# Kernel optimization log

Measured on AMD Instinct MI355X. Metric: run time of the kernel, lower is better.

Reference implementation:

```python
import jax, jax.numpy as jnp
import numpy as np

N_AGENTS = 12
N_THREADS = 4096
DIM = 3
N_VEC = 4
HID = 64
INV_NF = 32
LAYERS = 2
N = N_THREADS * N_AGENTS


def _intra_graph_edges():
    # fully-connected directed edges within each env's agent graph
    i, j = np.meshgrid(np.arange(N_AGENTS), np.arange(N_AGENTS), indexing='ij')
    mask = i != j
    ri, ci = i[mask], j[mask]  # [132]
    off = (np.arange(N_THREADS) * N_AGENTS)[:, None]
    row = (ri[None, :] + off).reshape(-1).astype(np.int32)
    col = (ci[None, :] + off).reshape(-1).astype(np.int32)
    return jnp.asarray(row), jnp.asarray(col)


def setup_inputs() -> dict:
    key = jax.random.key(0)
    ks = jax.random.split(key, 16)
    s = 0.05
    row, col = _intra_graph_edges()
    return {
        'h0': jax.random.normal(ks[0], (N, INV_NF), jnp.float32),
        'x0': jax.random.normal(ks[1], (N, DIM, N_VEC), jnp.float32),
        'W_embed': jax.random.normal(ks[2], (INV_NF, HID), jnp.float32) * s,
        'b_embed': jnp.zeros((HID,), jnp.float32),
        'We1': jax.random.normal(ks[3], (LAYERS, 2 * HID + N_VEC, HID), jnp.float32) * s,
        'be1': jnp.zeros((LAYERS, HID), jnp.float32),
        'We2': jax.random.normal(ks[4], (LAYERS, HID, HID), jnp.float32) * s,
        'be2': jnp.zeros((LAYERS, HID), jnp.float32),
        'Wx': jax.random.normal(ks[5], (LAYERS, HID, N_VEC), jnp.float32) * s,
        'bx': jnp.zeros((LAYERS, N_VEC), jnp.float32),
        'Wh1': jax.random.normal(ks[6], (LAYERS, 2 * HID, HID), jnp.float32) * s,
        'bh1': jnp.zeros((LAYERS, HID), jnp.float32),
        'Wh2': jax.random.normal(ks[7], (LAYERS, HID, HID), jnp.float32) * s,
        'bh2': jnp.zeros((LAYERS, HID), jnp.float32),
        'w_act': jax.random.normal(ks[8], (N_VEC,), jnp.float32) * s,
        'log_std': jnp.full((DIM,), -0.5, jnp.float32),
        'row': row,
        'col': col,
    }


def reference(h0, x0, W_embed, b_embed, We1, be1, We2, be2, Wx, bx,
              Wh1, bh1, Wh2, bh2, w_act, log_std, row, col):
    silu = jax.nn.silu
    n = h0.shape[0]
    h = h0 @ W_embed + b_embed            # node embedding, [N, HID]
    x = x0                                 # equivariant features, [N, DIM, N_VEC]
    deg = jnp.maximum(jax.ops.segment_sum(jnp.ones_like(row, jnp.float32), row, num_segments=n), 1.0)
    for l in range(LAYERS):
        hi, hj = h[row], h[col]
        diff = x[row] - x[col]                        # [E, DIM, N_VEC]
        radial = jnp.sum(diff * diff, axis=1)          # [E, N_VEC]
        m = silu(jnp.concatenate([hi, hj, radial], -1) @ We1[l] + be1[l])
        m = silu(m @ We2[l] + be2[l])                  # edge messages [E, HID]
        wc = m @ Wx[l] + bx[l]                         # per-vector coord weights [E, N_VEC]
        x = x + jax.ops.segment_sum(diff * wc[:, None, :], row, num_segments=n) / deg[:, None, None]
        agg = jax.ops.segment_sum(m, row, num_segments=n)
        h = h + silu(jnp.concatenate([h, agg], -1) @ Wh1[l] + bh1[l]) @ Wh2[l] + bh2[l]
    mu = jnp.einsum('ndv,v->nd', x, w_act)             # act_net: Linear(N_VEC,1,bias=False)
    actions = mu                                        # deterministic: mode of Normal(mu, std)
    log_probs = jnp.broadcast_to(-log_std - 0.5 * jnp.log(2.0 * jnp.pi), mu.shape)
    actions = actions.reshape(N_THREADS, N_AGENTS, DIM)
    log_probs = log_probs.reshape(N_THREADS, N_AGENTS, DIM)
    return actions, log_probs
```

## Files before the change

### kernel.cpp

```cpp
#include <hip/hip_runtime.h>

#define NAG 12
#define NTH 4096
#define NEDGE 132
#define ENVW 4
#define LDB 72
#define LDT 20

typedef __bf16 bf16_8 __attribute__((ext_vector_type(8)));
typedef __bf16 bf16_4 __attribute__((ext_vector_type(4)));
typedef float  f32x4  __attribute__((ext_vector_type(4)));

#define MFMA(a,b,c) __builtin_amdgcn_mfma_f32_16x16x32_bf16((a),(b),(c),0,0,0)

#define WS_FRAGS 100
#define WS_BIAS_F32 25600
#define WS_BX_F32   27648
#define WS_BYTES 111104

__device__ __forceinline__ float silu_f(float z) {
    float e = __expf(-z);
    return z * __builtin_amdgcn_rcpf(1.0f + e);
}

__device__ __forceinline__ bf16_8 loadB64(const float* __restrict__ W, int kbase, int n, int q) {
    bf16_8 b;
    #pragma unroll
    for (int j = 0; j < 8; ++j) b[j] = (__bf16)W[(kbase + q*8 + j) * 64 + n];
    return b;
}

__device__ __forceinline__ bf16_8 packA8(const float* S) {
    f32x4 u = *(const f32x4*)S, v = *(const f32x4*)(S + 4);
    bf16_8 a;
    a[0]=(__bf16)u.x; a[1]=(__bf16)u.y; a[2]=(__bf16)u.z; a[3]=(__bf16)u.w;
    a[4]=(__bf16)v.x; a[5]=(__bf16)v.y; a[6]=(__bf16)v.z; a[7]=(__bf16)v.w;
    return a;
}

__global__ __launch_bounds__(64) void prep_frags(
    const float* __restrict__ W_embed, const float* __restrict__ We1,
    const float* __restrict__ We2, const float* __restrict__ Wh1,
    const float* __restrict__ Wh2,
    const float* __restrict__ be1, const float* __restrict__ be2,
    const float* __restrict__ bh1, const float* __restrict__ bh2,
    const float* __restrict__ bx, __bf16* __restrict__ wsb)
{
    const int f = blockIdx.x, lane = threadIdx.x;
    const int q = lane >> 4, n16 = lane & 15;
    float* wsf = (float*)wsb;
    if (f < WS_FRAGS) {
        const float* src; int kbase, nbase;
        if (f < 4) { src = W_embed; kbase = 0; nbase = f * 16; }
        else {
            int g0 = f - 4, l = g0 / 48, r = g0 % 48;
            if      (r < 8)  { int nt=r>>1, kh=r&1;            src = We1 + l*NEDGE*64; kbase = kh*32;      nbase = nt*16; }
            else if (r < 16) { int rr=r-8,  nt=rr>>1, kh=rr&1; src = We1 + l*NEDGE*64; kbase = 64 + kh*32; nbase = nt*16; }
            else if (r < 24) { int rr=r-16, nt=rr>>1, kh=rr&1; src = We2 + l*64*64;    kbase = kh*32;      nbase = nt*16; }
            else if (r < 40) { int rr=r-24, nt=rr>>2, ks=rr&3; src = Wh1 + l*128*64;   kbase = ks*32;      nbase = nt*16; }
            else             { int rr=r-40, nt=rr>>1, kh=rr&1; src = Wh2 + l*64*64;    kbase = kh*32;      nbase = nt*16; }
        }
        bf16_8 b = loadB64(src, kbase, nbase + n16, q);
        *(bf16_8*)(wsb + (size_t)f * 512 + lane * 8) = b;
    } else if (f < WS_FRAGS + 8) {
        int f2 = f - WS_FRAGS, l = f2 >> 2, w = f2 & 3;
        const float* src = (w == 0 ? be1 : w == 1 ? be2 : w == 2 ? bh1 : bh2) + l * 64;
        f32x4 v = { src[n16], src[16 + n16], src[32 + n16], src[48 + n16] };
        *(f32x4*)(wsf + WS_BIAS_F32 + ((size_t)(l*4 + w) * 64 + lane) * 4) = v;
    } else {
        #pragma unroll
        for (int l = 0; l < 2; ++l)
            wsf[WS_BX_F32 + l*64 + lane] = (n16 < 4) ? bx[l*4 + n16] : 0.f;
    }
}

template<bool WS>
__device__ __forceinline__ bf16_8 frg(const __bf16* __restrict__ wsb, int fid,
                                      const float* __restrict__ src, int kbase, int n, int lane) {
    if (WS) return *(const bf16_8*)(wsb + (size_t)fid * 512 + lane * 8);
    else    return loadB64(src, kbase, n, (lane >> 4));
}

template<bool WS>
__global__ void __launch_bounds__(64) egnn11(
    const float* __restrict__ h0, const float* __restrict__ x0,
    const float* __restrict__ W_embed, const float* __restrict__ b_embed,
    const float* __restrict__ We1, const float* __restrict__ be1,
    const float* __restrict__ We2, const float* __restrict__ be2,
    const float* __restrict__ Wx, const float* __restrict__ bx,
    const float* __restrict__ Wh1, const float* __restrict__ bh1,
    const float* __restrict__ Wh2, const float* __restrict__ bh2,
    const float* __restrict__ w_act, const float* __restrict__ log_std,
    const __bf16* __restrict__ wsb, float* __restrict__ out)
{
    __shared__ __align__(16) __bf16 sh  [ENVW][NAG * LDB];
    __shared__ __align__(16) __bf16 sHa [ENVW][NAG * LDB];
    __shared__ __align__(16) __bf16 sHb [ENVW][NAG * LDB];
    __shared__ __align__(16) __bf16 mstT[ENVW][64 * LDT];
    __shared__ __align__(16) float  sx  [ENVW][NAG * 16];
    __shared__ __align__(16) __bf16 sWcB[ENVW][NEDGE * 4];
    __shared__ __align__(16) float  sWb [4 * 64];

    const int lane = threadIdx.x;
    const int q = lane >> 4, n16 = lane & 15;
    const int rowA = (n16 < NAG) ? n16 : (NAG - 1);
    const int env0 = blockIdx.x * ENVW;
    const float* wsf = (const float*)wsb;

    if (lane < NAG * 3) {
        int d = lane % 3;
        float lp = -log_std[d] - 0.9189385332046727f;
        #pragma unroll
        for (int ep = 0; ep < ENVW; ++ep)
            out[NTH * NAG * 3 + (env0 + ep) * (NAG*3) + lane] = lp;
    }

    #pragma unroll
    for (int p = 0; p < (ENVW * 144 + 63) / 64; ++p) {
        int idx = p * 64 + lane;
        if (idx < ENVW * 144) {
            int ep = idx / 144, r2 = idx - ep * 144;
            sx[ep][(r2 / 12) * 16 + r2 % 12] = x0[(env0) * NAG * 12 + idx];
        }
    }

    f32x4 hC[ENVW][4];
    {
        bf16_8 a[ENVW];
        #pragma unroll
        for (int ep = 0; ep < ENVW; ++ep)
            a[ep] = packA8(h0 + ((env0 + ep) * NAG + rowA) * 32 + q * 8);
        #pragma unroll
        for (int nt = 0; nt < 4; ++nt) {
            bf16_8 b = frg<WS>(wsb, nt, W_embed, 0, nt*16 + n16, lane);
            float bias = b_embed[nt*16 + n16];
            #pragma unroll
            for (int ep = 0; ep < ENVW; ++ep) {
                f32x4 acc = {0.f,0.f,0.f,0.f};
                acc = MFMA(a[ep], b, acc);
                #pragma unroll
                for (int r = 0; r < 4; ++r) acc[r] += bias;
                hC[ep][nt] = acc;
            }
        }
        #pragma unroll
        for (int ep = 0; ep < ENVW; ++ep)
            #pragma unroll
            for (int nt = 0; nt < 4; ++nt)
                #pragma unroll
                for (int r = 0; r < 4; ++r) {
                    int row = q*4 + r;
                    if (row < NAG) sh[ep][row*LDB + nt*16 + n16] = (__bf16)hC[ep][nt][r];
                }
    }

    #pragma unroll 1
    for (int l = 0; l < 2; ++l) {
        const float* We1l = We1 + l * NEDGE * 64;
        const float* be1l = be1 + l * 64;
        const float* be2l = be2 + l * 64;
        const float* Wxl  = Wx  + l * 64 * 4;
        const float* bxl  = bx  + l * 4;
        const float* We2l = We2 + l * 64 * 64;
        const float* Wh1l = Wh1 + l * 128 * 64;
        const float* bh1l = bh1 + l * 64;
        const float* Wh2l = Wh2 + l * 64 * 64;
        const float* bh2l = bh2 + l * 64;
        const int L = 4 + l * 48;

        f32x4 be1q, be2q, bh1q, bh2q;
        float bxv;
        if (WS) {
            const float* bb = wsf + WS_BIAS_F32 + (size_t)(l*4) * 256 + lane * 4;
            be1q = *(const f32x4*)(bb);
            be2q = *(const f32x4*)(bb + 256);
            bh1q = *(const f32x4*)(bb + 512);
            bh2q = *(const f32x4*)(bb + 768);
            bxv  = wsf[WS_BX_F32 + l*64 + lane];
        } else {
            #pragma unroll
            for (int nt = 0; nt < 4; ++nt) {
                be1q[nt] = be1l[nt*16+n16]; be2q[nt] = be2l[nt*16+n16];
                bh1q[nt] = bh1l[nt*16+n16]; bh2q[nt] = bh2l[nt*16+n16];
            }
            bxv = (n16 < 4) ? bxl[n16] : 0.f;
        }

        {
            bf16_8 a0[ENVW], a1[ENVW];
            #pragma unroll
            for (int ep = 0; ep < ENVW; ++ep) {
                a0[ep] = *(const bf16_8*)(sh[ep] + rowA*LDB + q*8);
                a1[ep] = *(const bf16_8*)(sh[ep] + rowA*LDB + 32 + q*8);
            }
            #pragma unroll
            for (int nt = 0; nt < 4; ++nt) {
                bf16_8 b0 = frg<WS>(wsb, L+nt*2+0,   We1l, 0,  nt*16+n16, lane);
                bf16_8 b1 = frg<WS>(wsb, L+nt*2+1,   We1l, 32, nt*16+n16, lane);
                bf16_8 c0 = frg<WS>(wsb, L+8+nt*2+0, We1l, 64, nt*16+n16, lane);
                bf16_8 c1 = frg<WS>(wsb, L+8+nt*2+1, We1l, 96, nt*16+n16, lane);
                #pragma unroll
                for (int ep = 0; ep < ENVW; ++ep) {
                    f32x4 aA = {0.f,0.f,0.f,0.f}, aB = {0.f,0.f,0.f,0.f};
                    aA = MFMA(a0[ep], b0, aA); aA = MFMA(a1[ep], b1, aA);
                    aB = MFMA(a0[ep], c0, aB); aB = MFMA(a1[ep], c1, aB);
                    #pragma unroll
                    for (int r = 0; r < 4; ++r) {
                        int row = q*4 + r;
                        if (row < NAG) {
                            sHa[ep][row*LDB + nt*16+n16] = (__bf16)(aA[r] + be1q[nt]);
                            sHb[ep][row*LDB + nt*16+n16] = (__bf16)aB[r];
                        }
                    }
                }
            }
        }
        #pragma unroll
        for (int p = 0; p < 4; ++p) sWb[p*64 + lane] = We1l[(128+p)*64 + lane];

        float agg[ENVW][NAG];
        #pragma unroll
        for (int ep = 0; ep < ENVW; ++ep)
            #pragma unroll
            for (int i = 0; i < NAG; ++i) agg[ep][i] = 0.f;
        bf16_8 w2f[4][2], wxf[2];
        #pragma unroll
        for (int nt = 0; nt < 4; ++nt) {
            w2f[nt][0] = frg<WS>(wsb, L+16+nt*2+0, We2l, 0,  nt*16+n16, lane);
            w2f[nt][1] = frg<WS>(wsb, L+16+nt*2+1, We2l, 32, nt*16+n16, lane);
        }
        #pragma unroll
        for (int kh = 0; kh < 2; ++kh) {
            bf16_8 b;
            #pragma unroll
            for (int j2 = 0; j2 < 8; ++j2)
                b[j2] = (n16 < 4) ? (__bf16)Wxl[(kh*32 + q*8 + j2)*4 + n16] : (__bf16)0.f;
            wxf[kh] = b;
        }

        #pragma unroll
        for (int t = 0; t < 9; ++t) {
            const int e  = t*16 + n16;
            const int ec = (e < NEDGE) ? e : (NEDGE - 1);
            const int i  = ec / 11;
            const int jj = ec - i * 11;
            const int j  = jj + (jj >= i);
            bf16_8 af[ENVW][2];
            #pragma unroll
            for (int ep = 0; ep < ENVW; ++ep) {
                f32x4 rd = {0.f,0.f,0.f,0.f};
                #pragma unroll
                for (int d = 0; d < 3; ++d) {
                    f32x4 xi = *(const f32x4*)(sx[ep] + i*16 + d*4);
                    f32x4 xj = *(const f32x4*)(sx[ep] + j*16 + d*4);
                    f32x4 df = xi - xj;
                    rd += df * df;
                }
                #pragma unroll
                for (int kh = 0; kh < 2; ++kh) {
                    const int cb = kh*32 + q*8;
                    bf16_8 ha = *(const bf16_8*)(sHa[ep] + i*LDB + cb);
                    bf16_8 hb = *(const bf16_8*)(sHb[ep] + j*LDB + cb);
                    f32x4 wr0 = {0.f,0.f,0.f,0.f}, wr1 = {0.f,0.f,0.f,0.f};
                    #pragma unroll
                    for (int v = 0; v < 4; ++v) {
                        f32x4 wa = *(const f32x4*)(sWb + v*64 + cb);
                        f32x4 wb = *(const f32x4*)(sWb + v*64 + cb + 4);
                        wr0 += rd[v] * wa; wr1 += rd[v] * wb;
                    }
                    bf16_8 a;
                    #pragma unroll
                    for (int c = 0; c < 4; ++c)
                        a[c]   = (__bf16)silu_f((float)ha[c]   + (float)hb[c]   + wr0[c]);
                    #pragma unroll
                    for (int c = 0; c < 4; ++c)
                        a[4+c] = (__bf16)silu_f((float)ha[4+c] + (float)hb[4+c] + wr1[c]);
                    af[ep][kh] = a;
                }
            }
            #pragma unroll
            for (int ep = 0; ep < ENVW; ++ep) {
                __bf16* mT = &mstT[ep][0];
                #pragma unroll
                for (int nt = 0; nt < 4; ++nt) {
                    f32x4 acc = {0.f,0.f,0.f,0.f};
                    acc = MFMA(af[ep][0], w2f[nt][0], acc);
                    acc = MFMA(af[ep][1], w2f[nt][1], acc);
                    bf16_4 mv;
                    #pragma unroll
                    for (int r = 0; r < 4; ++r) mv[r] = (__bf16)silu_f(acc[r] + be2q[nt]);
                    *(bf16_4*)(mT + (nt*16 + n16)*LDT + q*4) = mv;
                }
            }
            #pragma unroll
            for (int ep = 0; ep < ENVW; ++ep) {
                const __bf16* mT = &mstT[ep][0];
                bf16_8 aw0, aw1;
                #pragma unroll
                for (int j2 = 0; j2 < 8; ++j2) {
                    aw0[j2] = mT[(q*8 + j2)*LDT + n16];
                    aw1[j2] = mT[(32 + q*8 + j2)*LDT + n16];
                }
                f32x4 acc = {0.f,0.f,0.f,0.f};
                acc = MFMA(aw0, wxf[0], acc);
                acc = MFMA(aw1, wxf[1], acc);
                if (n16 < 4) {
                    #pragma unroll
                    for (int r = 0; r < 4; ++r) {
                        int row = t*16 + q*4 + r;
                        if (row < NEDGE) sWcB[ep][row*4 + n16] = (__bf16)(acc[r] + bxv);
                    }
                }
            }
            #pragma unroll
            for (int ep = 0; ep < ENVW; ++ep) {
                const __bf16* mT = &mstT[ep][0];
                bf16_4 c0 = *(const bf16_4*)(mT + lane*LDT + 0);
                #pragma unroll
                for (int el = 0; el < 4; ++el) agg[ep][(t*16 + el)/11] += (float)c0[el];
                if (t < 8) {
                    bf16_4 c1 = *(const bf16_4*)(mT + lane*LDT + 4);
                    bf16_4 c2 = *(const bf16_4*)(mT + lane*LDT + 8);
                    bf16_4 c3 = *(const bf16_4*)(mT + lane*LDT + 12);
                    #pragma unroll
                    for (int el = 0; el < 4; ++el) {
                        agg[ep][(t*16 + 4  + el)/11] += (float)c1[el];
                        agg[ep][(t*16 + 8  + el)/11] += (float)c2[el];
                        agg[ep][(t*16 + 12 + el)/11] += (float)c3[el];
                    }
                }
            }
        }
        #pragma unroll
        for (int ep = 0; ep < ENVW; ++ep)
            #pragma unroll
            for (int i = 0; i < NAG; ++i) sHb[ep][i*LDB + lane] = (__bf16)agg[ep][i];

        float xn[ENVW][3];
        #pragma unroll
        for (int p = 0; p < 3; ++p) {
            int idx = p*64 + lane;
            int xi = idx / 12, dv = idx % 12, v = dv & 3;
            bool act = idx < 144;
            int xic = act ? xi : 0;
            #pragma unroll
            for (int ep = 0; ep < ENVW; ++ep) {
                float xiv = sx[ep][xic*16 + dv];
                float acc = 0.f;
                #pragma unroll
                for (int j2 = 0; j2 < NAG; ++j2) {
                    int e2 = xic*11 + j2 - (j2 > xic ? 1 : 0);
                    e2 = (e2 < NEDGE) ? e2 : (NEDGE - 1);
                    float term = (xiv - sx[ep][j2*16 + dv]) * (float)sWcB[ep][e2*4 + v];
                    acc += (j2 == xic) ? 0.f : term;
                }
                xn[ep][p] = act ? (xiv + acc * (1.0f / 11.0f)) : 0.f;
            }
        }
        {
            bf16_8 ah0[ENVW], ah1[ENVW], ag0[ENVW], ag1[ENVW];
            #pragma unroll
            for (int ep = 0; ep < ENVW; ++ep) {
                ah0[ep] = *(const bf16_8*)(sh[ep]  + rowA*LDB + q*8);
                ah1[ep] = *(const bf16_8*)(sh[ep]  + rowA*LDB + 32 + q*8);
                ag0[ep] = *(const bf16_8*)(sHb[ep] + rowA*LDB + q*8);
                ag1[ep] = *(const bf16_8*)(sHb[ep] + rowA*LDB + 32 + q*8);
            }
            #pragma unroll
            for (int nt = 0; nt < 4; ++nt) {
                bf16_8 b0 = frg<WS>(wsb, L+24+nt*4+0, Wh1l, 0,  nt*16+n16, lane);
                bf16_8 b1 = frg<WS>(wsb, L+24+nt*4+1, Wh1l, 32, nt*16+n16, lane);
                bf16_8 b2 = frg<WS>(wsb, L+24+nt*4+2, Wh1l, 64, nt*16+n16, lane);
                bf16_8 b3 = frg<WS>(wsb, L+24+nt*4+3, Wh1l, 96, nt*16+n16, lane);
                #pragma unroll
                for (int ep = 0; ep < ENVW; ++ep) {
                    f32x4 acc = {0.f,0.f,0.f,0.f};
                    acc = MFMA(ah0[ep], b0, acc); acc = MFMA(ah1[ep], b1, acc);
                    acc = MFMA(ag0[ep], b2, acc); acc = MFMA(ag1[ep], b3, acc);
                    #pragma unroll
                    for (int r = 0; r < 4; ++r) {
                        int row = q*4 + r;
                        if (row < NAG) sHa[ep][row*LDB + nt*16+n16] = (__bf16)silu_f(acc[r] + bh1q[nt]);
                    }
                }
            }
        }
        #pragma unroll
        for (int p = 0; p < 3; ++p) {
            int idx = p*64 + lane;
            if (idx < 144) {
                #pragma unroll
                for (int ep = 0; ep < ENVW; ++ep)
                    sx[ep][(idx/12)*16 + idx%12] = xn[ep][p];
            }
        }
        {
            bf16_8 at0[ENVW], at1[ENVW];
            #pragma unroll
            for (int ep = 0; ep < ENVW; ++ep) {
                at0[ep] = *(const bf16_8*)(sHa[ep] + rowA*LDB + q*8);
                at1[ep] = *(const bf16_8*)(sHa[ep] + rowA*LDB + 32 + q*8);
            }
            #pragma unroll
            for (int nt = 0; nt < 4; ++nt) {
                bf16_8 b0 = frg<WS>(wsb, L+40+nt*2+0, Wh2l, 0,  nt*16+n16, lane);
                bf16_8 b1 = frg<WS>(wsb, L+40+nt*2+1, Wh2l, 32, nt*16+n16, lane);
                #pragma unroll
                for (int ep = 0; ep < ENVW; ++ep) {
                    f32x4 acc = {0.f,0.f,0.f,0.f};
                    acc = MFMA(at0[ep], b0, acc);
                    acc = MFMA(at1[ep], b1, acc);
                    #pragma unroll
                    for (int r = 0; r < 4; ++r) hC[ep][nt][r] += acc[r] + bh2q[nt];
                }
            }
            #pragma unroll
            for (int ep = 0; ep < ENVW; ++ep)
                #pragma unroll
                for (int nt = 0; nt < 4; ++nt)
                    #pragma unroll
                    for (int r = 0; r < 4; ++r) {
                        int row = q*4 + r;
                        if (row < NAG) sh[ep][row*LDB + nt*16+n16] = (__bf16)hC[ep][nt][r];
                    }
        }
    }

    if (lane < NAG * 3) {
        int i = lane / 3, d = lane - i * 3;
        #pragma unroll
        for (int ep = 0; ep < ENVW; ++ep) {
            float mu = 0.f;
            #pragma unroll
            for (int v = 0; v < 4; ++v) mu += sx[ep][i*16 + d*4 + v] * w_act[v];
            out[(env0 + ep) * (NAG*3) + lane] = mu;
        }
    }
}

extern "C" void kernel_launch(void* const* d_in, const int* in_sizes, int n_in,
                              void* d_out, int out_size, void* d_ws, size_t ws_size,
                              hipStream_t stream) {
    const float* h0   = (const float*)d_in[0];
    const float* x0   = (const float*)d_in[1];
    const float* Wem  = (const float*)d_in[2];
    const float* bem  = (const float*)d_in[3];
    const float* We1  = (const float*)d_in[4];
    const float* be1  = (const float*)d_in[5];
    const float* We2  = (const float*)d_in[6];
    const float* be2  = (const float*)d_in[7];
    const float* Wx   = (const float*)d_in[8];
    const float* bx   = (const float*)d_in[9];
    const float* Wh1  = (const float*)d_in[10];
    const float* bh1  = (const float*)d_in[11];
    const float* Wh2  = (const float*)d_in[12];
    const float* bh2  = (const float*)d_in[13];
    const float* wact = (const float*)d_in[14];
    const float* lstd = (const float*)d_in[15];
    float* out = (float*)d_out;

    if (ws_size >= (size_t)WS_BYTES) {
        prep_frags<<<dim3(WS_FRAGS + 9), dim3(64), 0, stream>>>(
            Wem, We1, We2, Wh1, Wh2, be1, be2, bh1, bh2, bx, (__bf16*)d_ws);
        egnn11<true><<<dim3(NTH / ENVW), dim3(64), 0, stream>>>(
            h0, x0, Wem, bem, We1, be1, We2, be2, Wx, bx,
            Wh1, bh1, Wh2, bh2, wact, lstd, (const __bf16*)d_ws, out);
    } else {
        egnn11<false><<<dim3(NTH / ENVW), dim3(64), 0, stream>>>(
            h0, x0, Wem, bem, We1, be1, We2, be2, Wx, bx,
            Wh1, bh1, Wh2, bh2, wact, lstd, nullptr, out);
    }
}
```

Baseline: 247.3 us.

## Pack four independent waves per block, each handling two environments

```diff
diff --git a/kernel.cpp b/kernel.cpp
--- a/kernel.cpp
+++ b/kernel.cpp
@@ -3,7 +3,8 @@
 #define NAG 12
 #define NTH 4096
 #define NEDGE 132
-#define ENVW 4
+#define ENVW 2
+#define NWAVE 4
 #define LDB 72
 #define LDT 20
 
@@ -82,7 +83,7 @@
 }
 
 template<bool WS>
-__global__ void __launch_bounds__(64) egnn11(
+__global__ void __launch_bounds__(64 * NWAVE) egnn11(
     const float* __restrict__ h0, const float* __restrict__ x0,
     const float* __restrict__ W_embed, const float* __restrict__ b_embed,
     const float* __restrict__ We1, const float* __restrict__ be1,
@@ -93,18 +94,20 @@
     const float* __restrict__ w_act, const float* __restrict__ log_std,
     const __bf16* __restrict__ wsb, float* __restrict__ out)
 {
-    __shared__ __align__(16) __bf16 sh  [ENVW][NAG * LDB];
-    __shared__ __align__(16) __bf16 sHa [ENVW][NAG * LDB];
-    __shared__ __align__(16) __bf16 sHb [ENVW][NAG * LDB];
-    __shared__ __align__(16) __bf16 mstT[ENVW][64 * LDT];
-    __shared__ __align__(16) float  sx  [ENVW][NAG * 16];
-    __shared__ __align__(16) __bf16 sWcB[ENVW][NEDGE * 4];
-    __shared__ __align__(16) float  sWb [4 * 64];
-
-    const int lane = threadIdx.x;
+    __shared__ __align__(16) __bf16 sh  [NWAVE][ENVW][NAG * LDB];
+    __shared__ __align__(16) __bf16 sHa [NWAVE][ENVW][NAG * LDB];
+    __shared__ __align__(16) __bf16 sHb [NWAVE][ENVW][NAG * LDB];
+    __shared__ __align__(16) __bf16 mstT[NWAVE][ENVW][64 * LDT];
+    __shared__ __align__(16) float  sx  [NWAVE][ENVW][NAG * 16];
+    __shared__ __align__(16) __bf16 sWcB[NWAVE][ENVW][NEDGE * 4];
+    __shared__ __align__(16) float  sWb [NWAVE][4 * 64];
+
+    const int tid  = threadIdx.x;
+    const int wv   = tid >> 6;
+    const int lane = tid & 63;
     const int q = lane >> 4, n16 = lane & 15;
     const int rowA = (n16 < NAG) ? n16 : (NAG - 1);
-    const int env0 = blockIdx.x * ENVW;
+    const int env0 = (blockIdx.x * NWAVE + wv) * ENVW;
     const float* wsf = (const float*)wsb;
 
     if (lane < NAG * 3) {
@@ -120,7 +123,7 @@
         int idx = p * 64 + lane;
         if (idx < ENVW * 144) {
             int ep = idx / 144, r2 = idx - ep * 144;
-            sx[ep][(r2 / 12) * 16 + r2 % 12] = x0[(env0) * NAG * 12 + idx];
+            sx[wv][ep][(r2 / 12) * 16 + r2 % 12] = x0[(env0) * NAG * 12 + idx];
         }
     }
 
@@ -150,7 +153,7 @@
                 #pragma unroll
                 for (int r = 0; r < 4; ++r) {
                     int row = q*4 + r;
-                    if (row < NAG) sh[ep][row*LDB + nt*16 + n16] = (__bf16)hC[ep][nt][r];
+                    if (row < NAG) sh[wv][ep][row*LDB + nt*16 + n16] = (__bf16)hC[ep][nt][r];
                 }
     }
 
@@ -190,8 +193,8 @@
             bf16_8 a0[ENVW], a1[ENVW];
             #pragma unroll
             for (int ep = 0; ep < ENVW; ++ep) {
-                a0[ep] = *(const bf16_8*)(sh[ep] + rowA*LDB + q*8);
-                a1[ep] = *(const bf16_8*)(sh[ep] + rowA*LDB + 32 + q*8);
+                a0[ep] = *(const bf16_8*)(sh[wv][ep] + rowA*LDB + q*8);
+                a1[ep] = *(const bf16_8*)(sh[wv][ep] + rowA*LDB + 32 + q*8);
             }
             #pragma unroll
             for (int nt = 0; nt < 4; ++nt) {
@@ -208,15 +211,15 @@
                     for (int r = 0; r < 4; ++r) {
                         int row = q*4 + r;
                         if (row < NAG) {
-                            sHa[ep][row*LDB + nt*16+n16] = (__bf16)(aA[r] + be1q[nt]);
-                            sHb[ep][row*LDB + nt*16+n16] = (__bf16)aB[r];
+                            sHa[wv][ep][row*LDB + nt*16+n16] = (__bf16)(aA[r] + be1q[nt]);
+                            sHb[wv][ep][row*LDB + nt*16+n16] = (__bf16)aB[r];
                         }
                     }
                 }
             }
         }
         #pragma unroll
-        for (int p = 0; p < 4; ++p) sWb[p*64 + lane] = We1l[(128+p)*64 + lane];
+        for (int p = 0; p < 4; ++p) sWb[wv][p*64 + lane] = We1l[(128+p)*64 + lane];
 
         float agg[ENVW][NAG];
         #pragma unroll
@@ -251,21 +254,21 @@
                 f32x4 rd = {0.f,0.f,0.f,0.f};
                 #pragma unroll
                 for (int d = 0; d < 3; ++d) {
-                    f32x4 xi = *(const f32x4*)(sx[ep] + i*16 + d*4);
-                    f32x4 xj = *(const f32x4*)(sx[ep] + j*16 + d*4);
+                    f32x4 xi = *(const f32x4*)(sx[wv][ep] + i*16 + d*4);
+                    f32x4 xj = *(const f32x4*)(sx[wv][ep] + j*16 + d*4);
                     f32x4 df = xi - xj;
                     rd += df * df;
                 }
                 #pragma unroll
                 for (int kh = 0; kh < 2; ++kh) {
                     const int cb = kh*32 + q*8;
-                    bf16_8 ha = *(const bf16_8*)(sHa[ep] + i*LDB + cb);
-                    bf16_8 hb = *(const bf16_8*)(sHb[ep] + j*LDB + cb);
+                    bf16_8 ha = *(const bf16_8*)(sHa[wv][ep] + i*LDB + cb);
+                    bf16_8 hb = *(const bf16_8*)(sHb[wv][ep] + j*LDB + cb);
                     f32x4 wr0 = {0.f,0.f,0.f,0.f}, wr1 = {0.f,0.f,0.f,0.f};
                     #pragma unroll
                     for (int v = 0; v < 4; ++v) {
-                        f32x4 wa = *(const f32x4*)(sWb + v*64 + cb);
-                        f32x4 wb = *(const f32x4*)(sWb + v*64 + cb + 4);
+                        f32x4 wa = *(const f32x4*)(sWb[wv] + v*64 + cb);
+                        f32x4 wb = *(const f32x4*)(sWb[wv] + v*64 + cb + 4);
                         wr0 += rd[v] * wa; wr1 += rd[v] * wb;
                     }
                     bf16_8 a;
@@ -280,7 +283,7 @@
             }
             #pragma unroll
             for (int ep = 0; ep < ENVW; ++ep) {
-                __bf16* mT = &mstT[ep][0];
+                __bf16* mT = &mstT[wv][ep][0];
                 #pragma unroll
                 for (int nt = 0; nt < 4; ++nt) {
                     f32x4 acc = {0.f,0.f,0.f,0.f};
@@ -294,7 +297,7 @@
             }
             #pragma unroll
             for (int ep = 0; ep < ENVW; ++ep) {
-                const __bf16* mT = &mstT[ep][0];
+                const __bf16* mT = &mstT[wv][ep][0];
                 bf16_8 aw0, aw1;
                 #pragma unroll
                 for (int j2 = 0; j2 < 8; ++j2) {
@@ -308,13 +311,13 @@
                     #pragma unroll
                     for (int r = 0; r < 4; ++r) {
                         int row = t*16 + q*4 + r;
-                        if (row < NEDGE) sWcB[ep][row*4 + n16] = (__bf16)(acc[r] + bxv);
-                    }
-                }
-            }
-            #pragma unroll
-            for (int ep = 0; ep < ENVW; ++ep) {
-                const __bf16* mT = &mstT[ep][0];
+                        if (row < NEDGE) sWcB[wv][ep][row*4 + n16] = (__bf16)(acc[r] + bxv);
+                    }
+                }
+            }
+            #pragma unroll
+            for (int ep = 0; ep < ENVW; ++ep) {
+                const __bf16* mT = &mstT[wv][ep][0];
                 bf16_4 c0 = *(const bf16_4*)(mT + lane*LDT + 0);
                 #pragma unroll
                 for (int el = 0; el < 4; ++el) agg[ep][(t*16 + el)/11] += (float)c0[el];
@@ -334,7 +337,7 @@
         #pragma unroll
         for (int ep = 0; ep < ENVW; ++ep)
             #pragma unroll
-            for (int i = 0; i < NAG; ++i) sHb[ep][i*LDB + lane] = (__bf16)agg[ep][i];
+            for (int i = 0; i < NAG; ++i) sHb[wv][ep][i*LDB + lane] = (__bf16)agg[ep][i];
 
         float xn[ENVW][3];
         #pragma unroll
@@ -345,13 +348,13 @@
             int xic = act ? xi : 0;
             #pragma unroll
             for (int ep = 0; ep < ENVW; ++ep) {
-                float xiv = sx[ep][xic*16 + dv];
+                float xiv = sx[wv][ep][xic*16 + dv];
                 float acc = 0.f;
                 #pragma unroll
                 for (int j2 = 0; j2 < NAG; ++j2) {
                     int e2 = xic*11 + j2 - (j2 > xic ? 1 : 0);
                     e2 = (e2 < NEDGE) ? e2 : (NEDGE - 1);
-                    float term = (xiv - sx[ep][j2*16 + dv]) * (float)sWcB[ep][e2*4 + v];
+                    float term = (xiv - sx[wv][ep][j2*16 + dv]) * (float)sWcB[wv][ep][e2*4 + v];
                     acc += (j2 == xic) ? 0.f : term;
                 }
                 xn[ep][p] = act ? (xiv + acc * (1.0f / 11.0f)) : 0.f;
@@ -361,10 +364,10 @@
             bf16_8 ah0[ENVW], ah1[ENVW], ag0[ENVW], ag1[ENVW];
             #pragma unroll
             for (int ep = 0; ep < ENVW; ++ep) {
-                ah0[ep] = *(const bf16_8*)(sh[ep]  + rowA*LDB + q*8);
-                ah1[ep] = *(const bf16_8*)(sh[ep]  + rowA*LDB + 32 + q*8);
-                ag0[ep] = *(const bf16_8*)(sHb[ep] + rowA*LDB + q*8);
-                ag1[ep] = *(const bf16_8*)(sHb[ep] + rowA*LDB + 32 + q*8);
+                ah0[ep] = *(const bf16_8*)(sh[wv][ep]  + rowA*LDB + q*8);
+                ah1[ep] = *(const bf16_8*)(sh[wv][ep]  + rowA*LDB + 32 + q*8);
+                ag0[ep] = *(const bf16_8*)(sHb[wv][ep] + rowA*LDB + q*8);
+                ag1[ep] = *(const bf16_8*)(sHb[wv][ep] + rowA*LDB + 32 + q*8);
             }
             #pragma unroll
             for (int nt = 0; nt < 4; ++nt) {
@@ -380,7 +383,7 @@
                     #pragma unroll
                     for (int r = 0; r < 4; ++r) {
                         int row = q*4 + r;
-                        if (row < NAG) sHa[ep][row*LDB + nt*16+n16] = (__bf16)silu_f(acc[r] + bh1q[nt]);
+                        if (row < NAG) sHa[wv][ep][row*LDB + nt*16+n16] = (__bf16)silu_f(acc[r] + bh1q[nt]);
                     }
                 }
             }
@@ -391,15 +394,15 @@
             if (idx < 144) {
                 #pragma unroll
                 for (int ep = 0; ep < ENVW; ++ep)
-                    sx[ep][(idx/12)*16 + idx%12] = xn[ep][p];
+                    sx[wv][ep][(idx/12)*16 + idx%12] = xn[ep][p];
             }
         }
         {
             bf16_8 at0[ENVW], at1[ENVW];
             #pragma unroll
             for (int ep = 0; ep < ENVW; ++ep) {
-                at0[ep] = *(const bf16_8*)(sHa[ep] + rowA*LDB + q*8);
-                at1[ep] = *(const bf16_8*)(sHa[ep] + rowA*LDB + 32 + q*8);
+                at0[ep] = *(const bf16_8*)(sHa[wv][ep] + rowA*LDB + q*8);
+                at1[ep] = *(const bf16_8*)(sHa[wv][ep] + rowA*LDB + 32 + q*8);
             }
             #pragma unroll
             for (int nt = 0; nt < 4; ++nt) {
@@ -421,7 +424,7 @@
                     #pragma unroll
                     for (int r = 0; r < 4; ++r) {
                         int row = q*4 + r;
-                        if (row < NAG) sh[ep][row*LDB + nt*16+n16] = (__bf16)hC[ep][nt][r];
+                        if (row < NAG) sh[wv][ep][row*LDB + nt*16+n16] = (__bf16)hC[ep][nt][r];
                     }
         }
     }
@@ -432,7 +435,7 @@
         for (int ep = 0; ep < ENVW; ++ep) {
             float mu = 0.f;
             #pragma unroll
-            for (int v = 0; v < 4; ++v) mu += sx[ep][i*16 + d*4 + v] * w_act[v];
+            for (int v = 0; v < 4; ++v) mu += sx[wv][ep][i*16 + d*4 + v] * w_act[v];
             out[(env0 + ep) * (NAG*3) + lane] = mu;
         }
     }
@@ -462,11 +465,11 @@
     if (ws_size >= (size_t)WS_BYTES) {
         prep_frags<<<dim3(WS_FRAGS + 9), dim3(64), 0, stream>>>(
             Wem, We1, We2, Wh1, Wh2, be1, be2, bh1, bh2, bx, (__bf16*)d_ws);
-        egnn11<true><<<dim3(NTH / ENVW), dim3(64), 0, stream>>>(
+        egnn11<true><<<dim3(NTH / (ENVW * NWAVE)), dim3(64 * NWAVE), 0, stream>>>(
             h0, x0, Wem, bem, We1, be1, We2, be2, Wx, bx,
             Wh1, bh1, Wh2, bh2, wact, lstd, (const __bf16*)d_ws, out);
     } else {
-        egnn11<false><<<dim3(NTH / ENVW), dim3(64), 0, stream>>>(
+        egnn11<false><<<dim3(NTH / (ENVW * NWAVE)), dim3(64 * NWAVE), 0, stream>>>(
             h0, x0, Wem, bem, We1, be1, We2, be2, Wx, bx,
             Wh1, bh1, Wh2, bh2, wact, lstd, nullptr, out);
     }
```

After: 222.1 us. 10.2% less time.

## Split each block's work across two waves and aggregate messages via MFMA

Applied to the files above, without the earlier changes.

```diff
diff --git a/kernel.cpp b/kernel.cpp
--- a/kernel.cpp
+++ b/kernel.cpp
@@ -3,7 +3,8 @@
 #define NAG 12
 #define NTH 4096
 #define NEDGE 132
-#define ENVW 4
+#define ENVW 2
+#define WPB 2
 #define LDB 72
 #define LDT 20
 
@@ -13,10 +14,10 @@
 
 #define MFMA(a,b,c) __builtin_amdgcn_mfma_f32_16x16x32_bf16((a),(b),(c),0,0,0)
 
-#define WS_FRAGS 100
-#define WS_BIAS_F32 25600
-#define WS_BX_F32   27648
-#define WS_BYTES 111104
+#define WS_FRAGS 109
+#define WS_BIAS_F32 27904
+#define WS_BX_F32   29952
+#define WS_BYTES 120320
 
 __device__ __forceinline__ float silu_f(float z) {
     float e = __expf(-z);
@@ -32,6 +33,13 @@
 
 __device__ __forceinline__ bf16_8 packA8(const float* S) {
     f32x4 u = *(const f32x4*)S, v = *(const f32x4*)(S + 4);
+    bf16_8 a;
+    a[0]=(__bf16)u.x; a[1]=(__bf16)u.y; a[2]=(__bf16)u.z; a[3]=(__bf16)u.w;
+    a[4]=(__bf16)v.x; a[5]=(__bf16)v.y; a[6]=(__bf16)v.z; a[7]=(__bf16)v.w;
+    return a;
+}
+
+__device__ __forceinline__ bf16_8 packA8v(f32x4 u, f32x4 v) {
     bf16_8 a;
     a[0]=(__bf16)u.x; a[1]=(__bf16)u.y; a[2]=(__bf16)u.z; a[3]=(__bf16)u.w;
     a[4]=(__bf16)v.x; a[5]=(__bf16)v.y; a[6]=(__bf16)v.z; a[7]=(__bf16)v.w;
@@ -49,7 +57,7 @@
     const int f = blockIdx.x, lane = threadIdx.x;
     const int q = lane >> 4, n16 = lane & 15;
     float* wsf = (float*)wsb;
-    if (f < WS_FRAGS) {
+    if (f < 100) {
         const float* src; int kbase, nbase;
         if (f < 4) { src = W_embed; kbase = 0; nbase = f * 16; }
         else {
@@ -62,6 +70,16 @@
         }
         bf16_8 b = loadB64(src, kbase, nbase + n16, q);
         *(bf16_8*)(wsb + (size_t)f * 512 + lane * 8) = b;
+    } else if (f < WS_FRAGS) {
+        int t = f - 100;
+        bf16_8 b;
+        #pragma unroll
+        for (int j = 0; j < 8; ++j) {
+            int k = q * 8 + j;
+            int e = t * 16 + k;
+            b[j] = (k < 16 && e < NEDGE && (e / 11) == n16) ? (__bf16)1.0f : (__bf16)0.0f;
+        }
+        *(bf16_8*)(wsb + (size_t)f * 512 + lane * 8) = b;
     } else if (f < WS_FRAGS + 8) {
         int f2 = f - WS_FRAGS, l = f2 >> 2, w = f2 & 3;
         const float* src = (w == 0 ? be1 : w == 1 ? be2 : w == 2 ? bh1 : bh2) + l * 64;
@@ -82,7 +100,7 @@
 }
 
 template<bool WS>
-__global__ void __launch_bounds__(64) egnn11(
+__global__ void __launch_bounds__(64 * WPB) egnn15(
     const float* __restrict__ h0, const float* __restrict__ x0,
     const float* __restrict__ W_embed, const float* __restrict__ b_embed,
     const float* __restrict__ We1, const float* __restrict__ be1,
@@ -96,42 +114,46 @@
     __shared__ __align__(16) __bf16 sh  [ENVW][NAG * LDB];
     __shared__ __align__(16) __bf16 sHa [ENVW][NAG * LDB];
     __shared__ __align__(16) __bf16 sHb [ENVW][NAG * LDB];
-    __shared__ __align__(16) __bf16 mstT[ENVW][64 * LDT];
+    __shared__ __align__(16) __bf16 mst [WPB][ENVW][64 * LDT];
+    __shared__ __align__(16) float  sAg [WPB][ENVW][NAG * 64];
     __shared__ __align__(16) float  sx  [ENVW][NAG * 16];
     __shared__ __align__(16) __bf16 sWcB[ENVW][NEDGE * 4];
     __shared__ __align__(16) float  sWb [4 * 64];
 
-    const int lane = threadIdx.x;
+    const int tid  = threadIdx.x;
+    const int wv   = tid >> 6;
+    const int lane = tid & 63;
     const int q = lane >> 4, n16 = lane & 15;
     const int rowA = (n16 < NAG) ? n16 : (NAG - 1);
     const int env0 = blockIdx.x * ENVW;
     const float* wsf = (const float*)wsb;
 
-    if (lane < NAG * 3) {
-        int d = lane % 3;
+    if (tid < NAG * 3) {
+        int d = tid % 3;
         float lp = -log_std[d] - 0.9189385332046727f;
         #pragma unroll
         for (int ep = 0; ep < ENVW; ++ep)
-            out[NTH * NAG * 3 + (env0 + ep) * (NAG*3) + lane] = lp;
+            out[NTH * NAG * 3 + (env0 + ep) * (NAG*3) + tid] = lp;
     }
 
     #pragma unroll
-    for (int p = 0; p < (ENVW * 144 + 63) / 64; ++p) {
-        int idx = p * 64 + lane;
+    for (int p = 0; p < 3; ++p) {
+        int idx = p * 128 + tid;
         if (idx < ENVW * 144) {
             int ep = idx / 144, r2 = idx - ep * 144;
             sx[ep][(r2 / 12) * 16 + r2 % 12] = x0[(env0) * NAG * 12 + idx];
         }
     }
 
-    f32x4 hC[ENVW][4];
+    f32x4 hC[ENVW][2];
     {
         bf16_8 a[ENVW];
         #pragma unroll
         for (int ep = 0; ep < ENVW; ++ep)
             a[ep] = packA8(h0 + ((env0 + ep) * NAG + rowA) * 32 + q * 8);
         #pragma unroll
-        for (int nt = 0; nt < 4; ++nt) {
+        for (int nt2 = 0; nt2 < 2; ++nt2) {
+            int nt = wv * 2 + nt2;
             bf16_8 b = frg<WS>(wsb, nt, W_embed, 0, nt*16 + n16, lane);
             float bias = b_embed[nt*16 + n16];
             #pragma unroll
@@ -140,19 +162,20 @@
                 acc = MFMA(a[ep], b, acc);
                 #pragma unroll
                 for (int r = 0; r < 4; ++r) acc[r] += bias;
-                hC[ep][nt] = acc;
+                hC[ep][nt2] = acc;
             }
         }
         #pragma unroll
         for (int ep = 0; ep < ENVW; ++ep)
             #pragma unroll
-            for (int nt = 0; nt < 4; ++nt)
+            for (int nt2 = 0; nt2 < 2; ++nt2)
                 #pragma unroll
                 for (int r = 0; r < 4; ++r) {
                     int row = q*4 + r;
-                    if (row < NAG) sh[ep][row*LDB + nt*16 + n16] = (__bf16)hC[ep][nt][r];
-                }
-    }
+                    if (row < NAG) sh[ep][row*LDB + (wv*2+nt2)*16 + n16] = (__bf16)hC[ep][nt2][r];
+                }
+    }
+    __syncthreads();
 
     #pragma unroll 1
     for (int l = 0; l < 2; ++l) {
@@ -168,20 +191,28 @@
         const float* bh2l = bh2 + l * 64;
         const int L = 4 + l * 48;
 
-        f32x4 be1q, be2q, bh1q, bh2q;
-        float bxv;
+        f32x4 be2q;
+        float be1s[2], bh1s[2], bh2s[2], bxv;
         if (WS) {
             const float* bb = wsf + WS_BIAS_F32 + (size_t)(l*4) * 256 + lane * 4;
-            be1q = *(const f32x4*)(bb);
             be2q = *(const f32x4*)(bb + 256);
-            bh1q = *(const f32x4*)(bb + 512);
-            bh2q = *(const f32x4*)(bb + 768);
-            bxv  = wsf[WS_BX_F32 + l*64 + lane];
+            #pragma unroll
+            for (int nt2 = 0; nt2 < 2; ++nt2) {
+                int nt = wv*2 + nt2;
+                be1s[nt2] = bb[nt];
+                bh1s[nt2] = bb[512 + nt];
+                bh2s[nt2] = bb[768 + nt];
+            }
+            bxv = wsf[WS_BX_F32 + l*64 + lane];
         } else {
             #pragma unroll
-            for (int nt = 0; nt < 4; ++nt) {
-                be1q[nt] = be1l[nt*16+n16]; be2q[nt] = be2l[nt*16+n16];
-                bh1q[nt] = bh1l[nt*16+n16]; bh2q[nt] = bh2l[nt*16+n16];
+            for (int nt = 0; nt < 4; ++nt) be2q[nt] = be2l[nt*16+n16];
+            #pragma unroll
+            for (int nt2 = 0; nt2 < 2; ++nt2) {
+                int nt = wv*2 + nt2;
+                be1s[nt2] = be1l[nt*16+n16];
+                bh1s[nt2] = bh1l[nt*16+n16];
+                bh2s[nt2] = bh2l[nt*16+n16];
             }
             bxv = (n16 < 4) ? bxl[n16] : 0.f;
         }
@@ -194,7 +225,8 @@
                 a1[ep] = *(const bf16_8*)(sh[ep] + rowA*LDB + 32 + q*8);
             }
             #pragma unroll
-            for (int nt = 0; nt < 4; ++nt) {
+            for (int nt2 = 0; nt2 < 2; ++nt2) {
+                int nt = wv*2 + nt2;
                 bf16_8 b0 = frg<WS>(wsb, L+nt*2+0,   We1l, 0,  nt*16+n16, lane);
                 bf16_8 b1 = frg<WS>(wsb, L+nt*2+1,   We1l, 32, nt*16+n16, lane);
                 bf16_8 c0 = frg<WS>(wsb, L+8+nt*2+0, We1l, 64, nt*16+n16, lane);
@@ -208,7 +240,7 @@
                     for (int r = 0; r < 4; ++r) {
                         int row = q*4 + r;
                         if (row < NAG) {
-                            sHa[ep][row*LDB + nt*16+n16] = (__bf16)(aA[r] + be1q[nt]);
+                            sHa[ep][row*LDB + nt*16+n16] = (__bf16)(aA[r] + be1s[nt2]);
                             sHb[ep][row*LDB + nt*16+n16] = (__bf16)aB[r];
                         }
                     }
@@ -216,13 +248,17 @@
             }
         }
         #pragma unroll
-        for (int p = 0; p < 4; ++p) sWb[p*64 + lane] = We1l[(128+p)*64 + lane];
-
-        float agg[ENVW][NAG];
+        for (int p2 = 0; p2 < 2; ++p2) {
+            int p = wv*2 + p2;
+            sWb[p*64 + lane] = We1l[(128+p)*64 + lane];
+        }
+        __syncthreads();
+
+        f32x4 aggC[ENVW][4];
         #pragma unroll
         for (int ep = 0; ep < ENVW; ++ep)
             #pragma unroll
-            for (int i = 0; i < NAG; ++i) agg[ep][i] = 0.f;
+            for (int nt = 0; nt < 4; ++nt) aggC[ep][nt] = (f32x4){0.f,0.f,0.f,0.f};
         bf16_8 w2f[4][2], wxf[2];
         #pragma unroll
         for (int nt = 0; nt < 4; ++nt) {
@@ -238,14 +274,14 @@
             wxf[kh] = b;
         }
 
-        #pragma unroll
-        for (int t = 0; t < 9; ++t) {
+        #pragma unroll 1
+        for (int t = (wv ? 4 : 0); t < (wv ? 9 : 4); ++t) {
             const int e  = t*16 + n16;
             const int ec = (e < NEDGE) ? e : (NEDGE - 1);
             const int i  = ec / 11;
             const int jj = ec - i * 11;
             const int j  = jj + (jj >= i);
-            bf16_8 af[ENVW][2];
+            f32x4 rdv[ENVW];
             #pragma unroll
             for (int ep = 0; ep < ENVW; ++ep) {
                 f32x4 rd = {0.f,0.f,0.f,0.f};
@@ -256,17 +292,26 @@
                     f32x4 df = xi - xj;
                     rd += df * df;
                 }
-                #pragma unroll
-                for (int kh = 0; kh < 2; ++kh) {
-                    const int cb = kh*32 + q*8;
+                rdv[ep] = rd;
+            }
+            bf16_8 af[ENVW][2];
+            #pragma unroll
+            for (int kh = 0; kh < 2; ++kh) {
+                const int cb = kh*32 + q*8;
+                f32x4 wa[4], wb[4];
+                #pragma unroll
+                for (int v = 0; v < 4; ++v) {
+                    wa[v] = *(const f32x4*)(sWb + v*64 + cb);
+                    wb[v] = *(const f32x4*)(sWb + v*64 + cb + 4);
+                }
+                #pragma unroll
+                for (int ep = 0; ep < ENVW; ++ep) {
                     bf16_8 ha = *(const bf16_8*)(sHa[ep] + i*LDB + cb);
                     bf16_8 hb = *(const bf16_8*)(sHb[ep] + j*LDB + cb);
                     f32x4 wr0 = {0.f,0.f,0.f,0.f}, wr1 = {0.f,0.f,0.f,0.f};
                     #pragma unroll
                     for (int v = 0; v < 4; ++v) {
-                        f32x4 wa = *(const f32x4*)(sWb + v*64 + cb);
-                        f32x4 wb = *(const f32x4*)(sWb + v*64 + cb + 4);
-                        wr0 += rd[v] * wa; wr1 += rd[v] * wb;
+                        wr0 += rdv[ep][v] * wa[v]; wr1 += rdv[ep][v] * wb[v];
                     }
                     bf16_8 a;
                     #pragma unroll
@@ -280,7 +325,7 @@
             }
             #pragma unroll
             for (int ep = 0; ep < ENVW; ++ep) {
-                __bf16* mT = &mstT[ep][0];
+                __bf16* mT = &mst[wv][ep][0];
                 #pragma unroll
                 for (int nt = 0; nt < 4; ++nt) {
                     f32x4 acc = {0.f,0.f,0.f,0.f};
@@ -294,7 +339,7 @@
             }
             #pragma unroll
             for (int ep = 0; ep < ENVW; ++ep) {
-                const __bf16* mT = &mstT[ep][0];
+                const __bf16* mT = &mst[wv][ep][0];
                 bf16_8 aw0, aw1;
                 #pragma unroll
                 for (int j2 = 0; j2 < 8; ++j2) {
@@ -312,34 +357,44 @@
                     }
                 }
             }
-            #pragma unroll
-            for (int ep = 0; ep < ENVW; ++ep) {
-                const __bf16* mT = &mstT[ep][0];
-                bf16_4 c0 = *(const bf16_4*)(mT + lane*LDT + 0);
-                #pragma unroll
-                for (int el = 0; el < 4; ++el) agg[ep][(t*16 + el)/11] += (float)c0[el];
-                if (t < 8) {
-                    bf16_4 c1 = *(const bf16_4*)(mT + lane*LDT + 4);
-                    bf16_4 c2 = *(const bf16_4*)(mT + lane*LDT + 8);
-                    bf16_4 c3 = *(const bf16_4*)(mT + lane*LDT + 12);
-                    #pragma unroll
-                    for (int el = 0; el < 4; ++el) {
-                        agg[ep][(t*16 + 4  + el)/11] += (float)c1[el];
-                        agg[ep][(t*16 + 8  + el)/11] += (float)c2[el];
-                        agg[ep][(t*16 + 12 + el)/11] += (float)c3[el];
-                    }
+            bf16_8 sfr;
+            if (WS) {
+                sfr = *(const bf16_8*)(wsb + (size_t)(100 + t) * 512 + lane * 8);
+            } else {
+                #pragma unroll
+                for (int j2 = 0; j2 < 8; ++j2) {
+                    int k = q*8 + j2, e2 = t*16 + k;
+                    sfr[j2] = (k < 16 && e2 < NEDGE && (e2 / 11) == n16) ? (__bf16)1.0f : (__bf16)0.0f;
+                }
+            }
+            #pragma unroll
+            for (int ep = 0; ep < ENVW; ++ep) {
+                const __bf16* mT = &mst[wv][ep][0];
+                #pragma unroll
+                for (int nt = 0; nt < 4; ++nt) {
+                    bf16_8 mb;
+                    #pragma unroll
+                    for (int c = 0; c < 8; ++c) mb[c] = (__bf16)0.f;
+                    if (q < 2) mb = *(const bf16_8*)(mT + (nt*16 + n16)*LDT + q*8);
+                    aggC[ep][nt] = MFMA(sfr, mb, aggC[ep][nt]);
                 }
             }
         }
         #pragma unroll
         for (int ep = 0; ep < ENVW; ++ep)
             #pragma unroll
-            for (int i = 0; i < NAG; ++i) sHb[ep][i*LDB + lane] = (__bf16)agg[ep][i];
-
-        float xn[ENVW][3];
-        #pragma unroll
-        for (int p = 0; p < 3; ++p) {
-            int idx = p*64 + lane;
+            for (int nt = 0; nt < 4; ++nt)
+                #pragma unroll
+                for (int r = 0; r < 4; ++r) {
+                    int row = q*4 + r;
+                    if (row < NAG) sAg[wv][ep][row*64 + nt*16+n16] = aggC[ep][nt][r];
+                }
+        __syncthreads();
+
+        float xn[ENVW][2];
+        #pragma unroll
+        for (int p = 0; p < 2; ++p) {
+            int idx = p*128 + tid;
             int xi = idx / 12, dv = idx % 12, v = dv & 3;
             bool act = idx < 144;
             int xic = act ? xi : 0;
@@ -361,13 +416,20 @@
             bf16_8 ah0[ENVW], ah1[ENVW], ag0[ENVW], ag1[ENVW];
             #pragma unroll
             for (int ep = 0; ep < ENVW; ++ep) {
-                ah0[ep] = *(const bf16_8*)(sh[ep]  + rowA*LDB + q*8);
-                ah1[ep] = *(const bf16_8*)(sh[ep]  + rowA*LDB + 32 + q*8);
-                ag0[ep] = *(const bf16_8*)(sHb[ep] + rowA*LDB + q*8);
-                ag1[ep] = *(const bf16_8*)(sHb[ep] + rowA*LDB + 32 + q*8);
-            }
-            #pragma unroll
-            for (int nt = 0; nt < 4; ++nt) {
+                ah0[ep] = *(const bf16_8*)(sh[ep] + rowA*LDB + q*8);
+                ah1[ep] = *(const bf16_8*)(sh[ep] + rowA*LDB + 32 + q*8);
+                const float* g0 = sAg[0][ep] + rowA*64;
+                const float* g1 = sAg[1][ep] + rowA*64;
+                f32x4 u0 = *(const f32x4*)(g0 + q*8)      + *(const f32x4*)(g1 + q*8);
+                f32x4 v0 = *(const f32x4*)(g0 + q*8 + 4)  + *(const f32x4*)(g1 + q*8 + 4);
+                f32x4 u1 = *(const f32x4*)(g0 + 32 + q*8) + *(const f32x4*)(g1 + 32 + q*8);
+                f32x4 v1 = *(const f32x4*)(g0 + 36 + q*8) + *(const f32x4*)(g1 + 36 + q*8);
+                ag0[ep] = packA8v(u0, v0);
+                ag1[ep] = packA8v(u1, v1);
+            }
+            #pragma unroll
+            for (int nt2 = 0; nt2 < 2; ++nt2) {
+                int nt = wv*2 + nt2;
                 bf16_8 b0 = frg<WS>(wsb, L+24+nt*4+0, Wh1l, 0,  nt*16+n16, lane);
                 bf16_8 b1 = frg<WS>(wsb, L+24+nt*4+1, Wh1l, 32, nt*16+n16, lane);
                 bf16_8 b2 = frg<WS>(wsb, L+24+nt*4+2, Wh1l, 64, nt*16+n16, lane);
@@ -380,14 +442,16 @@
                     #pragma unroll
                     for (int r = 0; r < 4; ++r) {
                         int row = q*4 + r;
-                        if (row < NAG) sHa[ep][row*LDB + nt*16+n16] = (__bf16)silu_f(acc[r] + bh1q[nt]);
+                        if (row < NAG) sHa[ep][row*LDB + nt*16+n16] = (__bf16)silu_f(acc[r] + bh1s[nt2]);
                     }
                 }
             }
         }
-        #pragma unroll
-        for (int p = 0; p < 3; ++p) {
-            int idx = p*64 + lane;
+        __syncthreads();
+
+        #pragma unroll
+        for (int p = 0; p < 2; ++p) {
+            int idx = p*128 + tid;
             if (idx < 144) {
                 #pragma unroll
                 for (int ep = 0; ep < ENVW; ++ep)
@@ -402,7 +466,8 @@
                 at1[ep] = *(const bf16_8*)(sHa[ep] + rowA*LDB + 32 + q*8);
             }
             #pragma unroll
-            for (int nt = 0; nt < 4; ++nt) {
+            for (int nt2 = 0; nt2 < 2; ++nt2) {
+                int nt = wv*2 + nt2;
                 bf16_8 b0 = frg<WS>(wsb, L+40+nt*2+0, Wh2l, 0,  nt*16+n16, lane);
                 bf16_8 b1 = frg<WS>(wsb, L+40+nt*2+1, Wh2l, 32, nt*16+n16, lane);
                 #pragma unroll
@@ -411,29 +476,30 @@
                     acc = MFMA(at0[ep], b0, acc);
                     acc = MFMA(at1[ep], b1, acc);
                     #pragma unroll
-                    for (int r = 0; r < 4; ++r) hC[ep][nt][r] += acc[r] + bh2q[nt];
+                    for (int r = 0; r < 4; ++r) hC[ep][nt2][r] += acc[r] + bh2s[nt2];
                 }
             }
             #pragma unroll
             for (int ep = 0; ep < ENVW; ++ep)
                 #pragma unroll
-                for (int nt = 0; nt < 4; ++nt)
+                for (int nt2 = 0; nt2 < 2; ++nt2)
                     #pragma unroll
                     for (int r = 0; r < 4; ++r) {
                         int row = q*4 + r;
-                        if (row < NAG) sh[ep][row*LDB + nt*16+n16] = (__bf16)hC[ep][nt][r];
+                        if (row < NAG) sh[ep][row*LDB + (wv*2+nt2)*16+n16] = (__bf16)hC[ep][nt2][r];
                     }
         }
-    }
-
-    if (lane < NAG * 3) {
-        int i = lane / 3, d = lane - i * 3;
+        __syncthreads();
+    }
+
+    if (tid < NAG * 3) {
+        int i = tid / 3, d = tid - i * 3;
         #pragma unroll
         for (int ep = 0; ep < ENVW; ++ep) {
             float mu = 0.f;
             #pragma unroll
             for (int v = 0; v < 4; ++v) mu += sx[ep][i*16 + d*4 + v] * w_act[v];
-            out[(env0 + ep) * (NAG*3) + lane] = mu;
+            out[(env0 + ep) * (NAG*3) + tid] = mu;
         }
     }
 }
@@ -462,11 +528,11 @@
     if (ws_size >= (size_t)WS_BYTES) {
         prep_frags<<<dim3(WS_FRAGS + 9), dim3(64), 0, stream>>>(
             Wem, We1, We2, Wh1, Wh2, be1, be2, bh1, bh2, bx, (__bf16*)d_ws);
-        egnn11<true><<<dim3(NTH / ENVW), dim3(64), 0, stream>>>(
+        egnn15<true><<<dim3(NTH / ENVW), dim3(64 * WPB), 0, stream>>>(
             h0, x0, Wem, bem, We1, be1, We2, be2, Wx, bx,
             Wh1, bh1, Wh2, bh2, wact, lstd, (const __bf16*)d_ws, out);
     } else {
-        egnn11<false><<<dim3(NTH / ENVW), dim3(64), 0, stream>>>(
+        egnn15<false><<<dim3(NTH / ENVW), dim3(64 * WPB), 0, stream>>>(
             h0, x0, Wem, bem, We1, be1, We2, be2, Wx, bx,
             Wh1, bh1, Wh2, bh2, wact, lstd, nullptr, out);
     }
```

New measurement: 262.2 us. +6.0%, slower.
